# Kernel optimization log

Hardware: AMD Instinct MI355X
Metric: run time of the kernel (lower is better)

## Reference

```python
import jax, jax.numpy as jnp
import numpy as np


def silu(v):
    return v * jax.nn.sigmoid(v)


def setup_inputs() -> dict:
    key = jax.random.key(0)
    ks = jax.random.split(key, 10)
    b, l, d_model = 1, 1024, 1536
    d_inner, dt_rank, d_state, d_conv = 3072, 96, 16, 4
    rn = lambda k, shp, sc: jax.random.normal(k, shp, jnp.float32) * sc
    return {
        "hidden_states": rn(ks[0], (b, l, d_model), 1.0),
        "in_proj_w": rn(ks[1], (2 * d_inner, d_model), 0.02),
        "conv_w": rn(ks[2], (d_inner, d_conv), 0.1),
        "conv_b": rn(ks[3], (d_inner,), 0.1),
        "x_proj_w": rn(ks[4], (dt_rank + 2 * d_state, d_inner), 0.02),
        "dt_proj_w": rn(ks[5], (d_inner, dt_rank), 0.02),
        "dt_proj_b": rn(ks[6], (d_inner,), 0.1),
        "out_proj_w": rn(ks[7], (d_model, d_inner), 0.02),
        "A_log": jnp.log(jax.random.uniform(ks[8], (d_inner, d_state), jnp.float32, 0.5, 8.0)),
        "D": rn(ks[9], (d_inner,), 1.0),
    }


def reference(hidden_states, in_proj_w, conv_w, conv_b, x_proj_w, dt_proj_w, dt_proj_b, out_proj_w, A_log, D):
    b, l, _ = hidden_states.shape
    d_inner, d_conv = conv_w.shape
    dt_rank = dt_proj_w.shape[1]
    d_state = A_log.shape[1]
    negA = -jnp.exp(A_log)  # (d_inner, d_state)

    # in_proj, transpose to channel-major: (b, 2*d_inner, l)
    xz = jnp.einsum('bld,ed->ble', hidden_states, in_proj_w).transpose(0, 2, 1)
    x, z = jnp.split(xz, 2, axis=1)  # each (b, d_inner, l)

    # conv_state = F.pad(x, (d_conv - l, 0)) -> last d_conv columns (l > d_conv)
    conv_state = x[:, :, -d_conv:]

    # causal depthwise conv1d + bias + silu
    xp = jnp.pad(x, ((0, 0), (0, 0), (d_conv - 1, 0)))
    xc = conv_b[None, :, None] + sum(conv_w[None, :, j:j + 1] * xp[:, :, j:j + l] for j in range(d_conv))
    xc = silu(xc)  # (b, d_inner, l)

    # x_proj over channel dim -> dt, B, C
    x_dbl = jnp.einsum('bdl,ed->ble', xc, x_proj_w)  # (b, l, dt_rank+2*d_state)
    dt, Bm, Cm = jnp.split(x_dbl, [dt_rank, dt_rank + d_state], axis=-1)

    # dt_proj (no bias here; bias folded into softplus as delta_bias)
    delta = jax.nn.softplus(jnp.einsum('blr,dr->bdl', dt, dt_proj_w) + dt_proj_b[None, :, None])

    # selective scan: h_t = exp(delta_t * A) * h_{t-1} + delta_t * B_t * x_t
    deltaA = jnp.exp(delta[..., None] * negA[None, :, None, :])          # (b, d, l, n)
    deltaBx = delta[..., None] * Bm[:, None, :, :] * xc[..., None]        # (b, d, l, n)

    def comb(c1, c2):
        a1, u1 = c1
        a2, u2 = c2
        return a1 * a2, a2 * u1 + u2

    _, h = jax.lax.associative_scan(comb, (deltaA, deltaBx), axis=2)      # (b, d, l, n)

    y = jnp.einsum('bdln,bln->bdl', h, Cm) + D[None, :, None] * xc
    y = y * silu(z)

    out = jnp.einsum('bdl,od->blo', y, out_proj_w)  # (b, l, d_model)
    last_state = h[:, :, -1, :]                     # (b, d_inner, d_state)
    return out, conv_state, last_state
```

## Files before the change

### kernel.cpp

```cpp
#include <hip/hip_runtime.h>

using f32x4  = __attribute__((ext_vector_type(4))) float;
using bf16x4 = __attribute__((ext_vector_type(4))) __bf16;
using bf16x8 = __attribute__((ext_vector_type(8))) __bf16;

#define L_SEQ 1024
#define D_MODEL 1536
#define D_INNER 3072
#define DT_RANK 96
#define D_STATE 16

#define SCAN_NC 32
#define SCAN_CL (L_SEQ / SCAN_NC)
#define NCHAIN  (D_INNER * D_STATE)

#define SCRATCH_FLOATS (4 * L_SEQ * D_INNER + L_SEQ * 128 + 3 * SCAN_NC * NCHAIN)
__device__ __align__(16) float g_scratch[SCRATCH_FLOATS];

template <int BM, int BN, int BK, int AMODE, int BMODE, int EPI, int SWZY = 0>
__global__ __launch_bounds__(256) void gemm_bt(
    const float* __restrict__ Ap, const float* __restrict__ Bp,
    float* __restrict__ out0, float* __restrict__ out1,
    const float* __restrict__ bias,
    int M, int N, int K, int lda, int ldb, int ldc)
{
    constexpr int LDSK = BK + 8;
    constexpr int WM = BM / 2, WN = BN / 2;
    constexpr int FM = WM / 16, FN = WN / 16;
    constexpr int CHA = (BM * BK / 256) / 4;
    constexpr int CHB = (BN * BK / 256) / 4;
    constexpr int CPR = BK / 4;
    __shared__ __align__(16) __bf16 As [BM * LDSK];
    __shared__ __align__(16) __bf16 As2[(AMODE == 2) ? BM * LDSK : 8];
    __shared__ __align__(16) __bf16 Bs [BN * LDSK];
    __shared__ __align__(16) __bf16 Bs2[(BMODE == 2) ? BN * LDSK : 8];

    const int tid  = threadIdx.x;
    const int lane = tid & 63;
    const int wid  = tid >> 6;
    const int wm = wid >> 1, wn = wid & 1;

    int m0, n0;
    if constexpr (SWZY > 0) {
        int b   = blockIdx.x;
        int xcd = b & 7;
        int j   = b >> 3;
        m0 = (j / SWZY) * BM;
        n0 = (xcd * SWZY + (j % SWZY)) * BN;
    } else {
        m0 = blockIdx.x * BM;
        n0 = blockIdx.y * BN;
    }

    const int nkt = (K + BK - 1) / BK;
    const int per = (nkt + (int)gridDim.z - 1) / (int)gridDim.z;
    const int kb  = blockIdx.z * per * BK;
    const int ke  = min(K, kb + per * BK);

    f32x4 acc[FM][FN];
#pragma unroll
    for (int i = 0; i < FM; ++i)
#pragma unroll
        for (int j = 0; j < FN; ++j) acc[i][j] = f32x4{0.f, 0.f, 0.f, 0.f};

    const int fr = lane & 15, kq = lane >> 4;

    f32x4 arg[CHA], brg[CHB];

    auto loadA = [&](int kt) {
#pragma unroll
        for (int i = 0; i < CHA; ++i) {
            int c = i * 256 + tid;
            int r = c / CPR, k4 = c % CPR;
            arg[i] = *(const f32x4*)(Ap + (size_t)(m0 + r) * lda + kt + k4 * 4);
        }
    };
    auto loadB = [&](int kt) {
#pragma unroll
        for (int i = 0; i < CHB; ++i) {
            int c = i * 256 + tid;
            int r = c / CPR, k4 = c % CPR;
            brg[i] = *(const f32x4*)(Bp + (size_t)(n0 + r) * ldb + kt + k4 * 4);
        }
    };
    auto writeA = [&]() {
#pragma unroll
        for (int i = 0; i < CHA; ++i) {
            int c = i * 256 + tid;
            int r = c / CPR, k4 = c % CPR;
            bf16x4 hv;
#pragma unroll
            for (int e = 0; e < 4; ++e) hv[e] = (__bf16)arg[i][e];
            *(bf16x4*)&As[r * LDSK + k4 * 4] = hv;
            if constexpr (AMODE == 2) {
                bf16x4 lv;
#pragma unroll
                for (int e = 0; e < 4; ++e)
                    lv[e] = (__bf16)(arg[i][e] - (float)hv[e]);
                *(bf16x4*)&As2[r * LDSK + k4 * 4] = lv;
            }
        }
    };
    auto writeB = [&]() {
#pragma unroll
        for (int i = 0; i < CHB; ++i) {
            int c = i * 256 + tid;
            int r = c / CPR, k4 = c % CPR;
            bf16x4 hv;
#pragma unroll
            for (int e = 0; e < 4; ++e) hv[e] = (__bf16)brg[i][e];
            *(bf16x4*)&Bs[r * LDSK + k4 * 4] = hv;
            if constexpr (BMODE == 2) {
                bf16x4 lv;
#pragma unroll
                for (int e = 0; e < 4; ++e)
                    lv[e] = (__bf16)(brg[i][e] - (float)hv[e]);
                *(bf16x4*)&Bs2[r * LDSK + k4 * 4] = lv;
            }
        }
    };

    loadA(kb);
    loadB(kb);

    for (int kt = kb; kt < ke; kt += BK) {
        writeA();
        writeB();
        __syncthreads();
        if (kt + BK < ke) {
            loadA(kt + BK);
            loadB(kt + BK);
        }
        bf16x8 af[FM], bfg[FN];
#pragma unroll
        for (int fm = 0; fm < FM; ++fm)
            af[fm] = *(const bf16x8*)&As[(wm * WM + fm * 16 + fr) * LDSK + kq * 8];
#pragma unroll
        for (int fn = 0; fn < FN; ++fn)
            bfg[fn] = *(const bf16x8*)&Bs[(wn * WN + fn * 16 + fr) * LDSK + kq * 8];
        if constexpr (AMODE == 2 && BMODE == 2) {
            bf16x8 al[FM], bl[FN];
#pragma unroll
            for (int fm = 0; fm < FM; ++fm)
                al[fm] = *(const bf16x8*)&As2[(wm * WM + fm * 16 + fr) * LDSK + kq * 8];
#pragma unroll
            for (int fn = 0; fn < FN; ++fn)
                bl[fn] = *(const bf16x8*)&Bs2[(wn * WN + fn * 16 + fr) * LDSK + kq * 8];
#pragma unroll
            for (int fm = 0; fm < FM; ++fm)
#pragma unroll
                for (int fn = 0; fn < FN; ++fn) {
                    acc[fm][fn] = __builtin_amdgcn_mfma_f32_16x16x32_bf16(
                        al[fm], bfg[fn], acc[fm][fn], 0, 0, 0);
                    acc[fm][fn] = __builtin_amdgcn_mfma_f32_16x16x32_bf16(
                        af[fm], bl[fn], acc[fm][fn], 0, 0, 0);
                    acc[fm][fn] = __builtin_amdgcn_mfma_f32_16x16x32_bf16(
                        af[fm], bfg[fn], acc[fm][fn], 0, 0, 0);
                }
        } else {
#pragma unroll
            for (int fm = 0; fm < FM; ++fm)
#pragma unroll
                for (int fn = 0; fn < FN; ++fn)
                    acc[fm][fn] = __builtin_amdgcn_mfma_f32_16x16x32_bf16(
                        af[fm], bfg[fn], acc[fm][fn], 0, 0, 0);
        }
        __syncthreads();
    }

    const int rbase = m0 + wm * WM, cbase = n0 + wn * WN;
#pragma unroll
    for (int fm = 0; fm < FM; ++fm) {
#pragma unroll
        for (int fn = 0; fn < FN; ++fn) {
            int row = rbase + fm * 16 + (lane >> 4) * 4;
            int col = cbase + fn * 16 + (lane & 15);
            f32x4 v = acc[fm][fn];
            if (EPI == 0) {
                int split = N / 2;
                float* d = (col < split) ? out0 : out1;
                int cc = (col < split) ? col : col - split;
#pragma unroll
                for (int j = 0; j < 4; ++j) d[(size_t)(row + j) * ldc + cc] = v[j];
            } else if (EPI == 1) {
                float bz = bias[col];
#pragma unroll
                for (int j = 0; j < 4; ++j) {
                    float t = v[j] + bz;
                    t = (t > 20.f) ? t : log1pf(__expf(t));
                    out0[(size_t)(row + j) * ldc + col] = t;
                }
            } else if (EPI == 2) {
#pragma unroll
                for (int j = 0; j < 4; ++j)
                    atomicAdd(&out0[(size_t)(row + j) * ldc + col], v[j]);
            } else if (EPI == 3) {
#pragma unroll
                for (int j = 0; j < 4; ++j)
                    out0[(size_t)(row + j) * ldc + col] = v[j];
            } else if (EPI == 4) {
                float* d = out0 + (size_t)blockIdx.z * M * ldc;
#pragma unroll
                for (int j = 0; j < 4; ++j)
                    d[(size_t)(row + j) * ldc + col] = v[j];
            } else {
#pragma unroll
                for (int j = 0; j < 4; ++j) {
                    float t = v[j] + bias[row + j];
                    t = (t > 20.f) ? t : log1pf(__expf(t));
                    out0[(size_t)(row + j) * ldc + col] = t;
                }
            }
        }
    }
}

__global__ __launch_bounds__(256) void zero_f32(float* __restrict__ p, int n4)
{
    int i = blockIdx.x * 256 + threadIdx.x;
    if (i < n4) ((f32x4*)p)[i] = f32x4{0.f, 0.f, 0.f, 0.f};
}

__global__ __launch_bounds__(256) void reduce2_f32(
    const float* __restrict__ p, float* __restrict__ out, int n4)
{
    int i = blockIdx.x * 256 + threadIdx.x;
    if (i < n4) {
        f32x4 a = ((const f32x4*)p)[i];
        f32x4 b = ((const f32x4*)(p + (size_t)L_SEQ * D_MODEL))[i];
        ((f32x4*)out)[i] = a + b;
    }
}

__global__ __launch_bounds__(256) void conv_silu(
    const float* __restrict__ x, const float* __restrict__ cw,
    const float* __restrict__ cb, float* __restrict__ xc,
    float* __restrict__ conv_state)
{
    int idx = blockIdx.x * 256 + threadIdx.x;
    int l  = idx / (D_INNER / 4);
    int d4 = (idx % (D_INNER / 4)) * 4;
    const f32x4 zero = f32x4{0.f, 0.f, 0.f, 0.f};
    f32x4 x0 = *(const f32x4*)&x[(size_t)l * D_INNER + d4];
    f32x4 x1 = (l >= 1) ? *(const f32x4*)&x[(size_t)(l - 1) * D_INNER + d4] : zero;
    f32x4 x2 = (l >= 2) ? *(const f32x4*)&x[(size_t)(l - 2) * D_INNER + d4] : zero;
    f32x4 x3 = (l >= 3) ? *(const f32x4*)&x[(size_t)(l - 3) * D_INNER + d4] : zero;
    f32x4 r;
#pragma unroll
    for (int i = 0; i < 4; ++i) {
        int d = d4 + i;
        float w0 = cw[d * 4 + 0], w1 = cw[d * 4 + 1];
        float w2 = cw[d * 4 + 2], w3 = cw[d * 4 + 3];
        float v = cb[d] + w3 * x0[i] + w2 * x1[i] + w1 * x2[i] + w0 * x3[i];
        r[i] = v / (1.f + __expf(-v));
    }
    *(f32x4*)&xc[(size_t)l * D_INNER + d4] = r;
    if (l == L_SEQ - 1) {
#pragma unroll
        for (int i = 0; i < 4; ++i) {
            int d = d4 + i;
            conv_state[d * 4 + 3] = x0[i];
            conv_state[d * 4 + 2] = x1[i];
            conv_state[d * 4 + 1] = x2[i];
            conv_state[d * 4 + 0] = x3[i];
        }
    }
}

__global__ __launch_bounds__(256) void scan_phase1(
    const float* __restrict__ delta, const float* __restrict__ xc,
    const float* __restrict__ dbl, const float* __restrict__ A_log,
    float* __restrict__ U, float* __restrict__ Aprod)
{
    int d = blockIdx.x * 256 + threadIdx.x;
    int c = blockIdx.y;
    float a[D_STATE], h[D_STATE], p[D_STATE];
#pragma unroll
    for (int n = 0; n < D_STATE; n += 4) {
        f32x4 av = *(const f32x4*)&A_log[d * D_STATE + n];
#pragma unroll
        for (int e = 0; e < 4; ++e) {
            a[n + e] = __expf(av[e]);
            h[n + e] = 0.f;
            p[n + e] = 1.f;
        }
    }
    int l0 = c * SCAN_CL;
    for (int i = 0; i < SCAN_CL; ++i) {
        int l = l0 + i;
        float dl = delta[(size_t)l * D_INNER + d];
        float xv = xc[(size_t)l * D_INNER + d];
        const float* Bp = dbl + l * 128 + DT_RANK;
        f32x4 B0 = *(const f32x4*)(Bp);
        f32x4 B1 = *(const f32x4*)(Bp + 4);
        f32x4 B2 = *(const f32x4*)(Bp + 8);
        f32x4 B3 = *(const f32x4*)(Bp + 12);
        float dx = dl * xv;
#pragma unroll
        for (int n = 0; n < D_STATE; ++n) {
            float Bv = (n < 4) ? B0[n] : (n < 8) ? B1[n - 4]
                     : (n < 12) ? B2[n - 8] : B3[n - 12];
            float dA = __expf(-dl * a[n]);
            h[n] = fmaf(dA, h[n], dx * Bv);
            p[n] *= dA;
        }
    }
    size_t base = (size_t)c * NCHAIN + (size_t)d * D_STATE;
#pragma unroll
    for (int n = 0; n < D_STATE; n += 4) {
        *(f32x4*)&U[base + n]     = f32x4{h[n], h[n+1], h[n+2], h[n+3]};
        *(f32x4*)&Aprod[base + n] = f32x4{p[n], p[n+1], p[n+2], p[n+3]};
    }
}

__global__ __launch_bounds__(256) void scan_phase2(
    const float* __restrict__ U, const float* __restrict__ Aprod,
    float* __restrict__ Hin, float* __restrict__ last_state)
{
    int r = blockIdx.x * 256 + threadIdx.x;
    float hin = 0.f;
#pragma unroll
    for (int c = 0; c < SCAN_NC; ++c) {
        Hin[c * NCHAIN + r] = hin;
        hin = fmaf(Aprod[c * NCHAIN + r], hin, U[c * NCHAIN + r]);
    }
    last_state[r] = hin;
}

__global__ __launch_bounds__(256) void scan_phase3(
    const float* __restrict__ delta, const float* __restrict__ xc,
    const float* __restrict__ z, const float* __restrict__ dbl,
    const float* __restrict__ A_log, const float* __restrict__ Dp,
    const float* __restrict__ Hin, float* __restrict__ y)
{
    int d = blockIdx.x * 256 + threadIdx.x;
    int c = blockIdx.y;
    float a[D_STATE], h[D_STATE];
    size_t hbase = (size_t)c * NCHAIN + (size_t)d * D_STATE;
#pragma unroll
    for (int n = 0; n < D_STATE; n += 4) {
        f32x4 av = *(const f32x4*)&A_log[d * D_STATE + n];
        f32x4 hv = *(const f32x4*)&Hin[hbase + n];
#pragma unroll
        for (int e = 0; e < 4; ++e) {
            a[n + e] = __expf(av[e]);
            h[n + e] = hv[e];
        }
    }
    float Dv = Dp[d];
    int l0 = c * SCAN_CL;
    for (int i = 0; i < SCAN_CL; ++i) {
        int l = l0 + i;
        float dl = delta[(size_t)l * D_INNER + d];
        float xv = xc[(size_t)l * D_INNER + d];
        float zv = z[(size_t)l * D_INNER + d];
        const float* Bp = dbl + l * 128 + DT_RANK;
        f32x4 B0 = *(const f32x4*)(Bp);
        f32x4 B1 = *(const f32x4*)(Bp + 4);
        f32x4 B2 = *(const f32x4*)(Bp + 8);
        f32x4 B3 = *(const f32x4*)(Bp + 12);
        f32x4 C0 = *(const f32x4*)(Bp + 16);
        f32x4 C1 = *(const f32x4*)(Bp + 20);
        f32x4 C2 = *(const f32x4*)(Bp + 24);
        f32x4 C3 = *(const f32x4*)(Bp + 28);
        float dx = dl * xv;
        float yv = 0.f;
#pragma unroll
        for (int n = 0; n < D_STATE; ++n) {
            float Bv = (n < 4) ? B0[n] : (n < 8) ? B1[n - 4]
                     : (n < 12) ? B2[n - 8] : B3[n - 12];
            float Cv = (n < 4) ? C0[n] : (n < 8) ? C1[n - 4]
                     : (n < 12) ? C2[n - 8] : C3[n - 12];
            float dA = __expf(-dl * a[n]);
            h[n] = fmaf(dA, h[n], dx * Bv);
            yv = fmaf(h[n], Cv, yv);
        }
        float sz = zv / (1.f + __expf(-zv));
        y[(size_t)l * D_INNER + d] = (yv + Dv * xv) * sz;
    }
}

extern "C" void kernel_launch(void* const* d_in, const int* in_sizes, int n_in,
                              void* d_out, int out_size, void* d_ws, size_t ws_size,
                              hipStream_t stream)
{
    const float* hs    = (const float*)d_in[0];
    const float* Win   = (const float*)d_in[1];
    const float* cw    = (const float*)d_in[2];
    const float* cb    = (const float*)d_in[3];
    const float* Wx    = (const float*)d_in[4];
    const float* Wdt   = (const float*)d_in[5];
    const float* dtb   = (const float*)d_in[6];
    const float* Wout  = (const float*)d_in[7];
    const float* A_log = (const float*)d_in[8];
    const float* Dp    = (const float*)d_in[9];

    float* out        = (float*)d_out;
    float* conv_state = out + (size_t)L_SEQ * D_MODEL;
    float* last_state = conv_state + (size_t)D_INNER * 4;

    const size_t NEED = sizeof(float) * (size_t)SCRATCH_FLOATS;
    float* base;
    if (ws_size >= NEED) {
        base = (float*)d_ws;
    } else {
        void* sp = nullptr;
        hipGetSymbolAddress(&sp, HIP_SYMBOL(g_scratch));
        base = (float*)sp;
    }
    float* buf0 = base;
    float* buf1 = buf0 + (size_t)L_SEQ * D_INNER;
    float* buf2 = buf1 + (size_t)L_SEQ * D_INNER;
    float* buf3 = buf2 + (size_t)L_SEQ * D_INNER;
    float* dbl  = buf3 + (size_t)L_SEQ * D_INNER;
    float* Ubuf = dbl  + (size_t)L_SEQ * 128;
    float* Abuf = Ubuf + (size_t)SCAN_NC * NCHAIN;
    float* Hbuf = Abuf + (size_t)SCAN_NC * NCHAIN;

    zero_f32<<<dim3((L_SEQ * 128 / 4 + 255) / 256), 256, 0, stream>>>(dbl, L_SEQ * 128 / 4);

    gemm_bt<128, 64, 32, 1, 1, 0, 12><<<dim3(768), 256, 0, stream>>>(
        hs, Win, buf0, buf1, nullptr, L_SEQ, 2 * D_INNER, D_MODEL, D_MODEL, D_MODEL, D_INNER);

    conv_silu<<<dim3(L_SEQ * D_INNER / 4 / 256), 256, 0, stream>>>(buf0, cw, cb, buf2, conv_state);

    gemm_bt<128, 128, 32, 2, 2, 2><<<dim3(8, 1, 24), 256, 0, stream>>>(
        buf2, Wx, dbl, nullptr, nullptr, L_SEQ, 128, D_INNER, D_INNER, D_INNER, 128);

    gemm_bt<128, 64, 32, 2, 2, 1><<<dim3(8, 48, 1), 256, 0, stream>>>(
        dbl, Wdt, buf0, nullptr, dtb, L_SEQ, D_INNER, DT_RANK, 128, DT_RANK, D_INNER);

    scan_phase1<<<dim3(D_INNER / 256, SCAN_NC), 256, 0, stream>>>(
        buf0, buf2, dbl, A_log, Ubuf, Abuf);
    scan_phase2<<<dim3(NCHAIN / 256), 256, 0, stream>>>(
        Ubuf, Abuf, Hbuf, last_state);
    scan_phase3<<<dim3(D_INNER / 256, SCAN_NC), 256, 0, stream>>>(
        buf0, buf2, buf1, dbl, A_log, Dp, Hbuf, buf3);

    gemm_bt<64, 64, 32, 1, 1, 4><<<dim3(16, 24, 2), 256, 0, stream>>>(
        buf3, Wout, buf0, nullptr, nullptr, L_SEQ, D_MODEL, D_INNER, D_INNER, D_INNER, D_MODEL);
    reduce2_f32<<<dim3(L_SEQ * D_MODEL / 4 / 256), 256, 0, stream>>>(
        buf0, out, L_SEQ * D_MODEL / 4);
}
```

Baseline: 198.5 us.

## Prefetch two K-tiles ahead in GEMM and shrink M tiles for more blocks

```diff
diff --git a/kernel.cpp b/kernel.cpp
--- a/kernel.cpp
+++ b/kernel.cpp
@@ -65,72 +65,61 @@
 
     const int fr = lane & 15, kq = lane >> 4;
 
-    f32x4 arg[CHA], brg[CHB];
-
-    auto loadA = [&](int kt) {
+    f32x4 a0[CHA], a1[CHA], b0[CHB], b1[CHB];
+
+    auto loadAb = [&](int kt, f32x4 (&buf)[CHA]) {
 #pragma unroll
         for (int i = 0; i < CHA; ++i) {
             int c = i * 256 + tid;
             int r = c / CPR, k4 = c % CPR;
-            arg[i] = *(const f32x4*)(Ap + (size_t)(m0 + r) * lda + kt + k4 * 4);
+            buf[i] = *(const f32x4*)(Ap + (size_t)(m0 + r) * lda + kt + k4 * 4);
         }
     };
-    auto loadB = [&](int kt) {
+    auto loadBb = [&](int kt, f32x4 (&buf)[CHB]) {
 #pragma unroll
         for (int i = 0; i < CHB; ++i) {
             int c = i * 256 + tid;
             int r = c / CPR, k4 = c % CPR;
-            brg[i] = *(const f32x4*)(Bp + (size_t)(n0 + r) * ldb + kt + k4 * 4);
+            buf[i] = *(const f32x4*)(Bp + (size_t)(n0 + r) * ldb + kt + k4 * 4);
         }
     };
-    auto writeA = [&]() {
+    auto writeAb = [&](f32x4 (&buf)[CHA]) {
 #pragma unroll
         for (int i = 0; i < CHA; ++i) {
             int c = i * 256 + tid;
             int r = c / CPR, k4 = c % CPR;
             bf16x4 hv;
 #pragma unroll
-            for (int e = 0; e < 4; ++e) hv[e] = (__bf16)arg[i][e];
+            for (int e = 0; e < 4; ++e) hv[e] = (__bf16)buf[i][e];
             *(bf16x4*)&As[r * LDSK + k4 * 4] = hv;
             if constexpr (AMODE == 2) {
                 bf16x4 lv;
 #pragma unroll
                 for (int e = 0; e < 4; ++e)
-                    lv[e] = (__bf16)(arg[i][e] - (float)hv[e]);
+                    lv[e] = (__bf16)(buf[i][e] - (float)hv[e]);
                 *(bf16x4*)&As2[r * LDSK + k4 * 4] = lv;
             }
         }
     };
-    auto writeB = [&]() {
+    auto writeBb = [&](f32x4 (&buf)[CHB]) {
 #pragma unroll
         for (int i = 0; i < CHB; ++i) {
             int c = i * 256 + tid;
             int r = c / CPR, k4 = c % CPR;
             bf16x4 hv;
 #pragma unroll
-            for (int e = 0; e < 4; ++e) hv[e] = (__bf16)brg[i][e];
+            for (int e = 0; e < 4; ++e) hv[e] = (__bf16)buf[i][e];
             *(bf16x4*)&Bs[r * LDSK + k4 * 4] = hv;
             if constexpr (BMODE == 2) {
                 bf16x4 lv;
 #pragma unroll
                 for (int e = 0; e < 4; ++e)
-                    lv[e] = (__bf16)(brg[i][e] - (float)hv[e]);
+                    lv[e] = (__bf16)(buf[i][e] - (float)hv[e]);
                 *(bf16x4*)&Bs2[r * LDSK + k4 * 4] = lv;
             }
         }
     };
-
-    loadA(kb);
-    loadB(kb);
-
-    for (int kt = kb; kt < ke; kt += BK) {
-        writeA();
-        writeB();
-        __syncthreads();
-        if (kt + BK < ke) {
-            loadA(kt + BK);
-            loadB(kt + BK);
-        }
+    auto compute = [&]() {
         bf16x8 af[FM], bfg[FN];
 #pragma unroll
         for (int fm = 0; fm < FM; ++fm)
@@ -165,7 +154,36 @@
                     acc[fm][fn] = __builtin_amdgcn_mfma_f32_16x16x32_bf16(
                         af[fm], bfg[fn], acc[fm][fn], 0, 0, 0);
         }
+    };
+
+    loadAb(kb, a0);
+    loadBb(kb, b0);
+    if (kb + BK < ke) {
+        loadAb(kb + BK, a1);
+        loadBb(kb + BK, b1);
+    }
+
+    for (int kt = kb; kt < ke; kt += 2 * BK) {
+        writeAb(a0);
+        writeBb(b0);
         __syncthreads();
+        if (kt + 2 * BK < ke) {
+            loadAb(kt + 2 * BK, a0);
+            loadBb(kt + 2 * BK, b0);
+        }
+        compute();
+        __syncthreads();
+        if (kt + BK < ke) {
+            writeAb(a1);
+            writeBb(b1);
+            __syncthreads();
+            if (kt + 3 * BK < ke) {
+                loadAb(kt + 3 * BK, a1);
+                loadBb(kt + 3 * BK, b1);
+            }
+            compute();
+            __syncthreads();
+        }
     }
 
     const int rbase = m0 + wm * WM, cbase = n0 + wn * WN;
@@ -419,15 +437,15 @@
 
     zero_f32<<<dim3((L_SEQ * 128 / 4 + 255) / 256), 256, 0, stream>>>(dbl, L_SEQ * 128 / 4);
 
-    gemm_bt<128, 64, 32, 1, 1, 0, 12><<<dim3(768), 256, 0, stream>>>(
+    gemm_bt<64, 64, 32, 1, 1, 0, 12><<<dim3(1536), 256, 0, stream>>>(
         hs, Win, buf0, buf1, nullptr, L_SEQ, 2 * D_INNER, D_MODEL, D_MODEL, D_MODEL, D_INNER);
 
     conv_silu<<<dim3(L_SEQ * D_INNER / 4 / 256), 256, 0, stream>>>(buf0, cw, cb, buf2, conv_state);
 
-    gemm_bt<128, 128, 32, 2, 2, 2><<<dim3(8, 1, 24), 256, 0, stream>>>(
+    gemm_bt<64, 128, 32, 2, 2, 2><<<dim3(16, 1, 24), 256, 0, stream>>>(
         buf2, Wx, dbl, nullptr, nullptr, L_SEQ, 128, D_INNER, D_INNER, D_INNER, 128);
 
-    gemm_bt<128, 64, 32, 2, 2, 1><<<dim3(8, 48, 1), 256, 0, stream>>>(
+    gemm_bt<64, 64, 32, 2, 2, 1><<<dim3(16, 48), 256, 0, stream>>>(
         dbl, Wdt, buf0, nullptr, dtb, L_SEQ, D_INNER, DT_RANK, 128, DT_RANK, D_INNER);
 
     scan_phase1<<<dim3(D_INNER / 256, SCAN_NC), 256, 0, stream>>>(
```

After: 199.0 us. Within noise of the previous version (+0.3%).
